# Optimization experiments

Measured on AMD Instinct MI355X. Metric: run time of the kernel, lower is better.

Reference implementation:

```python
import jax, jax.numpy as jnp
import numpy as np

NEG = -1e30  # finite stand-in for -inf padding (avoids NaN in logsumexp grads)


def _gconv(A, x, aW, ab, uW, ub):
    # Gconv: A column-normalized (L1 over dim=-2), x -> relu(a_fc(x)), relu(u_fc(x))
    An = A / jnp.maximum(jnp.sum(jnp.abs(A), axis=1, keepdims=True), 1e-12)
    ax = jax.nn.relu(x @ aW + ab)          # [B,N,D_out]
    ux = jax.nn.relu(x @ uW + ub)          # [B,N,D_out]
    return jnp.einsum('bij,bjd->bid', An, ax) + ux


def _sinkhorn(s, n1, n2, max_iter, tau):
    # log-domain Sinkhorn with ragged row/col masks (dummy_row=False, no unmatch).
    # Assumes n1[b] <= n2[b] and s.shape: [B, N1, N2] with N2 >= N1 (no transposes).
    B, N1, N2 = s.shape
    row_valid = jnp.arange(N1)[None, :] < n1[:, None]            # [B,N1]
    col_valid = jnp.arange(N2)[None, :] < n2[:, None]            # [B,N2]
    mask = row_valid[:, :, None] & col_valid[:, None, :]         # [B,N1,N2]
    log_s = jnp.where(mask, s / tau, NEG)
    for i in range(max_iter):
        if i % 2 == 0:
            lse = jax.nn.logsumexp(log_s, axis=2, keepdims=True)   # row sums
            log_s = jnp.where(row_valid[:, :, None], log_s - lse, log_s)
        else:
            lse = jax.nn.logsumexp(log_s, axis=1, keepdims=True)   # col sums
            log_s = jnp.where(col_valid[:, None, :], log_s - lse, log_s)
    return jnp.exp(jnp.where(mask, log_s, NEG))  # invalid entries -> 0


def _affinity(e1, W, e2):
    # WeightedInnerProdAffinity: e1 @ W @ e2^T
    return jnp.einsum('bid,de,bje->bij', e1, W, e2)


def setup_inputs() -> dict:
    key = jax.random.key(0)
    ks = jax.random.split(key, 20)
    B, N, IN, HID, OUT = 64, 256, 1024, 2048, 2048
    f32 = jnp.float32
    inp = {
        'feat1': jax.random.normal(ks[0], (B, N, IN), f32),
        'feat2': jax.random.normal(ks[1], (B, N, IN), f32),
        'A1': jax.random.uniform(ks[2], (B, N, N), f32),
        'A2': jax.random.uniform(ks[3], (B, N, N), f32),
        'g0_aW': jax.random.normal(ks[4], (IN, HID), f32) / np.float32(np.sqrt(IN)),
        'g0_ab': jnp.zeros((HID,), f32),
        'g0_uW': jax.random.normal(ks[5], (IN, HID), f32) / np.float32(np.sqrt(IN)),
        'g0_ub': jnp.zeros((HID,), f32),
        'g1_aW': jax.random.normal(ks[6], (HID, OUT), f32) / np.float32(np.sqrt(HID)),
        'g1_ab': jnp.zeros((OUT,), f32),
        'g1_uW': jax.random.normal(ks[7], (HID, OUT), f32) / np.float32(np.sqrt(HID)),
        'g1_ub': jnp.zeros((OUT,), f32),
        'aff0_W': jax.random.normal(ks[8], (HID, HID), f32) / np.float32(HID),
        'aff1_W': jax.random.normal(ks[9], (OUT, OUT), f32) / np.float32(OUT),
        'cross_W': jax.random.normal(ks[10], (2 * HID, HID), f32) / np.float32(np.sqrt(2 * HID)),
        'cross_b': jnp.zeros((HID,), f32),
        'n1': jax.random.randint(ks[11], (B,), 192, N + 1, jnp.int32),
        'n2': jnp.full((B,), N, jnp.int32),
        'cross_iter_num': -1,
        'sk_max_iter': 10,
        'sk_tau': 1,
    }
    return inp


def reference(feat1, feat2, A1, A2,
              g0_aW, g0_ab, g0_uW, g0_ub,
              g1_aW, g1_ab, g1_uW, g1_ub,
              aff0_W, aff1_W, cross_W, cross_b,
              n1, n2, cross_iter_num, sk_max_iter, sk_tau):
    tau = float(sk_tau)
    # layer 0 (Siamese Gconv, shared weights)
    emb1 = _gconv(A1, feat1, g0_aW, g0_ab, g0_uW, g0_ub)
    emb2 = _gconv(A2, feat2, g0_aW, g0_ab, g0_uW, g0_ub)
    # cross-graph update at i == gnn_layer - 2 (== 0 for num_layers=2)
    s = _affinity(emb1, aff0_W, emb2)
    s = _sinkhorn(s, n1, n2, sk_max_iter, tau)
    new_emb1 = jnp.concatenate([emb1, jnp.einsum('bij,bjd->bid', s, emb2)], -1) @ cross_W + cross_b
    new_emb2 = jnp.concatenate([emb2, jnp.einsum('bji,bjd->bid', s, emb1)], -1) @ cross_W + cross_b
    # layer 1 (final Siamese Gconv)
    emb1 = _gconv(A1, new_emb1, g1_aW, g1_ab, g1_uW, g1_ub)
    emb2 = _gconv(A2, new_emb2, g1_aW, g1_ab, g1_uW, g1_ub)
    s = _affinity(emb1, aff1_W, emb2)
    return _sinkhorn(s, n1, n2, sk_max_iter, tau)
```

## Files before the change

### kernel.cpp

```cpp
#include <hip/hip_runtime.h>
#include <cstdint>
#include <cstddef>

typedef __bf16 bf16;
typedef float f32x4 __attribute__((ext_vector_type(4)));
typedef bf16  bf16x8 __attribute__((ext_vector_type(8)));

#define NEGV (-1e30f)

enum { EPI_STORE = 0, EPI_ADD = 1, EPI_BIAS_RELU = 2, EPI_BIAS = 3,
       EPI_STORE_T = 5, EPI_BIAS_RELU_SCALE_T = 6, EPI_PART = 7, EPI_PARTP = 8 };

__device__ __forceinline__ void gload16(const void* g, void* l) {
    __builtin_amdgcn_global_load_lds((const __attribute__((address_space(1))) void*)g,
                                     (__attribute__((address_space(3))) void*)l, 16, 0, 0);
}

template<int EPI, typename CT, int NTJ>
__global__ __launch_bounds__(256, 2)
void hgemm_k(const bf16* __restrict__ Ab, const bf16* __restrict__ Bb,
             CT* __restrict__ Cb, const int M, const int N, const int K,
             const long long sA, const long long sB, const long long sC,
             const long long sH, const float* __restrict__ bias)
{
    __shared__ bf16 Asl[128 * 32];
    __shared__ bf16 Bsl[NTJ * 32 * 32];
    const int bz = (int)blockIdx.z;
    int ba = bz, kbeg = 0, klen = K;
    long long aoff = 0;
    if constexpr (EPI == EPI_PART) {
        ba = bz >> 3;
        const int ks = bz & 7;
        kbeg = (ks & 3) * (K >> 2); klen = K >> 2;
        aoff = (long long)(ks >> 2) * sH;
    }
    if constexpr (EPI == EPI_PARTP) {
        ba = 0; kbeg = bz * (K >> 1); klen = K >> 1;
    }
    const bf16* __restrict__ A = Ab + (long long)ba * sA + aoff;
    const bf16* __restrict__ B = Bb + (long long)ba * sB;
    CT* __restrict__ C;
    if constexpr (EPI == EPI_PART)
        C = Cb + (long long)((bz & 7) * ((int)gridDim.z >> 3) + (bz >> 3)) * sC;
    else
        C = Cb + (long long)bz * sC;

    const int m0 = blockIdx.y * 128, n0 = blockIdx.x * (NTJ * 32);
    const int tid = (int)threadIdx.x;
    const int lane = tid & 63, wave = tid >> 6;
    const int wm = (wave & 1) * 64, wn = (wave >> 1) * (NTJ * 16);
    const int lrow = lane & 15, quad = lane >> 4;

    f32x4 acc[4][NTJ];
    const f32x4 zero = {0.f, 0.f, 0.f, 0.f};
#pragma unroll
    for (int i = 0; i < 4; ++i)
#pragma unroll
        for (int j = 0; j < NTJ; ++j) acc[i][j] = zero;

    const int sr = tid >> 2, sck = (tid & 3) * 8;
    const bf16* ga0 = A + (long long)(m0 + sr) * K + kbeg + sck;
    const bf16* ga1 = ga0 + (long long)64 * K;
    const bf16* gb0 = B + (long long)(n0 + sr) * K + kbeg + sck;
    const bf16* gb1 = gb0 + (long long)64 * K;
    bf16* la0 = Asl + tid * 8;
    bf16* la1 = Asl + 2048 + tid * 8;
    bf16* lb0 = Bsl + tid * 8;
    bf16* lb1 = Bsl + 2048 + tid * 8;
    const bf16* ar = Asl + (wm + lrow) * 32 + quad * 8;
    const bf16* br = Bsl + (wn + lrow) * 32 + quad * 8;

    for (int k0 = 0; k0 < klen; k0 += 32) {
        gload16(ga0, la0); gload16(ga1, la1);
        gload16(gb0, lb0);
        if constexpr (NTJ == 4) gload16(gb1, lb1);
        ga0 += 32; ga1 += 32; gb0 += 32; gb1 += 32;
        __syncthreads();
        bf16x8 af[4], bfr[NTJ];
#pragma unroll
        for (int t = 0; t < 4; ++t) af[t] = *(const bf16x8*)(ar + t * 512);
#pragma unroll
        for (int t = 0; t < NTJ; ++t) bfr[t] = *(const bf16x8*)(br + t * 512);
#pragma unroll
        for (int i = 0; i < 4; ++i)
#pragma unroll
            for (int j = 0; j < NTJ; ++j)
                acc[i][j] = __builtin_amdgcn_mfma_f32_16x16x32_bf16(af[i], bfr[j], acc[i][j], 0, 0, 0);
        __syncthreads();
    }

#pragma unroll
    for (int ti = 0; ti < 4; ++ti) {
        const int gm0 = m0 + wm + ti * 16 + quad * 4;
#pragma unroll
        for (int r = 0; r < 4; ++r) {
            const int gm = gm0 + r;
#pragma unroll
            for (int tj = 0; tj < NTJ; ++tj) {
                const int gn = n0 + wn + tj * 16 + lrow;
                const float v = acc[ti][tj][r];
                CT* cp = C + (size_t)gm * N + gn;
                if constexpr (EPI == EPI_STORE)          *cp = (CT)v;
                else if constexpr (EPI == EPI_PART)      *cp = (CT)v;
                else if constexpr (EPI == EPI_PARTP)     *cp = (CT)v;
                else if constexpr (EPI == EPI_ADD)       *cp = (CT)((float)*cp + v);
                else if constexpr (EPI == EPI_BIAS_RELU) *cp = (CT)fmaxf(v + bias[gn], 0.f);
                else if constexpr (EPI == EPI_BIAS)      *cp = (CT)(v + bias[gn]);
            }
        }
    }
}

template<int EPI0, int EPI1, bool SWAPA0>
__global__ __launch_bounds__(256, 2)
void hgemm2_k(const bf16* __restrict__ Ab,
              const bf16* __restrict__ B0b, const bf16* __restrict__ B1b,
              bf16* __restrict__ C0b, bf16* __restrict__ C1b,
              const int M, const int N, const int K,
              const long long sA, const long long sC0, const long long sC1,
              const long long sR,
              const float* __restrict__ bias0, const float* __restrict__ bias1,
              const float* __restrict__ rowscale)
{
    __shared__ bf16 Asl[128 * 32];
    __shared__ bf16 Bsl[128 * 32];
    const int bz = (int)blockIdx.z;
    const int g = bz & 1, wsel = bz >> 1;
    const int asel = (wsel == 0 && SWAPA0) ? (g ^ 1) : g;
    const bf16* __restrict__ A = Ab + (long long)asel * sA;
    const bf16* __restrict__ B = wsel ? B1b : B0b;
    bf16* __restrict__ C = wsel ? (C1b + (long long)g * sC1)
                                : (C0b + (long long)g * sC0);
    const float* __restrict__ bias = wsel ? bias1 : bias0;
    const float* __restrict__ rs = rowscale + (long long)g * sR;

    const int m0 = blockIdx.y * 128, n0 = blockIdx.x * 128;
    const int tid = (int)threadIdx.x;
    const int lane = tid & 63, wave = tid >> 6;
    const int wm = (wave & 1) * 64, wn = (wave >> 1) * 64;
    const int lrow = lane & 15, quad = lane >> 4;

    f32x4 acc[4][4];
    const f32x4 zero = {0.f, 0.f, 0.f, 0.f};
#pragma unroll
    for (int i = 0; i < 4; ++i)
#pragma unroll
        for (int j = 0; j < 4; ++j) acc[i][j] = zero;

    const int sr = tid >> 2, sck = (tid & 3) * 8;
    const bf16* ga0 = A + (long long)(m0 + sr) * K + sck;
    const bf16* ga1 = ga0 + (long long)64 * K;
    const bf16* gb0 = B + (long long)(n0 + sr) * K + sck;
    const bf16* gb1 = gb0 + (long long)64 * K;
    bf16* la0 = Asl + tid * 8;
    bf16* la1 = Asl + 2048 + tid * 8;
    bf16* lb0 = Bsl + tid * 8;
    bf16* lb1 = Bsl + 2048 + tid * 8;
    const bf16* ar = Asl + (wm + lrow) * 32 + quad * 8;
    const bf16* br = Bsl + (wn + lrow) * 32 + quad * 8;

    for (int k0 = 0; k0 < K; k0 += 32) {
        gload16(ga0, la0); gload16(ga1, la1);
        gload16(gb0, lb0); gload16(gb1, lb1);
        ga0 += 32; ga1 += 32; gb0 += 32; gb1 += 32;
        __syncthreads();
        bf16x8 af[4], bfr[4];
#pragma unroll
        for (int t = 0; t < 4; ++t) {
            af[t]  = *(const bf16x8*)(ar + t * 512);
            bfr[t] = *(const bf16x8*)(br + t * 512);
        }
#pragma unroll
        for (int i = 0; i < 4; ++i)
#pragma unroll
            for (int j = 0; j < 4; ++j)
                acc[i][j] = __builtin_amdgcn_mfma_f32_16x16x32_bf16(af[i], bfr[j], acc[i][j], 0, 0, 0);
        __syncthreads();
    }

    if (wsel == 0) {
#pragma unroll
        for (int ti = 0; ti < 4; ++ti) {
            const int gm0 = m0 + wm + ti * 16 + quad * 4;
#pragma unroll
            for (int tj = 0; tj < 4; ++tj) {
                const int gn = n0 + wn + tj * 16 + lrow;
                union { bf16 h[4]; uint2 u; } p;
#pragma unroll
                for (int r = 0; r < 4; ++r) {
                    float v = acc[ti][tj][r];
                    if constexpr (EPI0 == EPI_BIAS_RELU_SCALE_T)
                        v = fmaxf(v + bias[gn], 0.f) * rs[gm0 + r];
                    p.h[r] = (bf16)v;
                }
                *(uint2*)(C + ((size_t)(gm0 >> 8)) * 524288 +
                          (size_t)gn * 256 + (gm0 & 255)) = p.u;
            }
        }
    } else {
#pragma unroll
        for (int ti = 0; ti < 4; ++ti) {
            const int gm0 = m0 + wm + ti * 16 + quad * 4;
#pragma unroll
            for (int r = 0; r < 4; ++r) {
                const int gm = gm0 + r;
#pragma unroll
                for (int tj = 0; tj < 4; ++tj) {
                    const int gn = n0 + wn + tj * 16 + lrow;
                    const float v = acc[ti][tj][r];
                    bf16* cp = C + (size_t)gm * N + gn;
                    if constexpr (EPI1 == EPI_BIAS_RELU) *cp = (bf16)fmaxf(v + bias[gn], 0.f);
                    else                                 *cp = (bf16)(v + bias[gn]);
                }
            }
        }
    }
}

__global__ __launch_bounds__(256)
void wtrans_k(const float* __restrict__ W, bf16* __restrict__ Wt, const int K, const int N)
{
    __shared__ float tl[32][33];
    const int k0 = blockIdx.y * 32, n0 = blockIdx.x * 32;
    const int tx = (int)threadIdx.x & 31, ty = (int)threadIdx.x >> 5;
#pragma unroll
    for (int q = 0; q < 4; ++q)
        tl[ty + 8 * q][tx] = W[(size_t)(k0 + ty + 8 * q) * N + n0 + tx];
    __syncthreads();
#pragma unroll
    for (int q = 0; q < 4; ++q)
        Wt[(size_t)(n0 + ty + 8 * q) * K + k0 + tx] = (bf16)tl[tx][ty + 8 * q];
}

__global__ __launch_bounds__(256)
void cvt_k(const float4* __restrict__ in, uint2* __restrict__ out, const long long n4)
{
    long long i = (long long)blockIdx.x * 256 + threadIdx.x;
    const long long st = (long long)gridDim.x * 256;
    for (; i < n4; i += st) {
        const float4 v = in[i];
        union { bf16 h[4]; uint2 u; } p;
        p.h[0] = (bf16)v.x; p.h[1] = (bf16)v.y; p.h[2] = (bf16)v.z; p.h[3] = (bf16)v.w;
        out[i] = p.u;
    }
}

__global__ __launch_bounds__(256)
void colsum_rcp_k(const float* __restrict__ A, float* __restrict__ rcs,
                  const int nbl2, const int g)
{
    const int b = blockIdx.x, j = (int)threadIdx.x;
    const int cch = b >> nbl2, ii = b & ((1 << nbl2) - 1), nb = 1 << nbl2;
    const float* p = A + (size_t)b * 65536;
    float s = 0.f;
    for (int i = 0; i < 256; ++i) s += fabsf(p[i * 256 + j]);
    rcs[(size_t)((cch * 2 + g) * nb + ii) * 256 + j] = 1.f / fmaxf(s, 1e-12f);
}

__global__ __launch_bounds__(256)
void mask_tau_red_k(const float* __restrict__ Sp, float* __restrict__ S,
                    const int* __restrict__ n1p, const int* __restrict__ n2p,
                    const int* __restrict__ taup, const int nb)
{
    const size_t t = (size_t)blockIdx.x * 256 + threadIdx.x;
    const int b = (int)(t >> 16), i = (int)((t >> 8) & 255), j = (int)(t & 255);
    const size_t stride = (size_t)nb << 16;
    float s = 0.f;
#pragma unroll
    for (int ks = 0; ks < 8; ++ks) s += Sp[ks * stride + t];
    const float tau = (float)taup[0];
    S[t] = (i < n1p[b] && j < n2p[b]) ? s / tau : NEGV;
}

template<int WRITE_SB>
__global__ __launch_bounds__(1024, 4)
void sk_fused_k(float* __restrict__ S, bf16* __restrict__ S2b,
                const int* __restrict__ n1p, const int* __restrict__ n2p,
                const int nbl2)
{
    __shared__ float lm[32][256];
    __shared__ float lp[4][256];
    __shared__ float lf[256];
    const int b = (int)blockIdx.x;
    const int tid = (int)threadIdx.x;
    const int a = tid >> 5, bb = tid & 31;
    const int r0 = a * 8, c0 = bb * 8;
    const int n1 = n1p[b], n2 = n2p[b];
    float* Sb_ = S + ((size_t)b << 16);

    float v[8][8];
#pragma unroll
    for (int ri = 0; ri < 8; ++ri) {
        const float4* rp = (const float4*)(Sb_ + (size_t)(r0 + ri) * 256 + c0);
        const float4 x0 = rp[0], x1 = rp[1];
        v[ri][0] = x0.x; v[ri][1] = x0.y; v[ri][2] = x0.z; v[ri][3] = x0.w;
        v[ri][4] = x1.x; v[ri][5] = x1.y; v[ri][6] = x1.z; v[ri][7] = x1.w;
    }

    for (int it = 0; it < 10; ++it) {
        if ((it & 1) == 0) {
#pragma unroll
            for (int ri = 0; ri < 8; ++ri) {
                float m = v[ri][0];
#pragma unroll
                for (int c = 1; c < 8; ++c) m = fmaxf(m, v[ri][c]);
#pragma unroll
                for (int off = 1; off < 32; off <<= 1) m = fmaxf(m, __shfl_xor(m, off));
                float s = 0.f;
#pragma unroll
                for (int c = 0; c < 8; ++c) s += expf(v[ri][c] - m);
#pragma unroll
                for (int off = 1; off < 32; off <<= 1) s += __shfl_xor(s, off);
                const float lse = m + logf(s);
                if (r0 + ri < n1) {
#pragma unroll
                    for (int c = 0; c < 8; ++c) v[ri][c] -= lse;
                }
            }
        } else {
            __syncthreads();
#pragma unroll
            for (int c = 0; c < 8; ++c) {
                float m = v[0][c];
#pragma unroll
                for (int ri = 1; ri < 8; ++ri) m = fmaxf(m, v[ri][c]);
                lm[a][c0 + c] = m;
            }
            __syncthreads();
            {
                const int jt = tid & 255, qt = tid >> 8;
                float m = lm[qt * 8][jt];
#pragma unroll
                for (int aa = 1; aa < 8; ++aa) m = fmaxf(m, lm[qt * 8 + aa][jt]);
                lp[qt][jt] = m;
            }
            __syncthreads();
            if (tid < 256)
                lf[tid] = fmaxf(fmaxf(lp[0][tid], lp[1][tid]),
                                fmaxf(lp[2][tid], lp[3][tid]));
            __syncthreads();
            float M[8];
#pragma unroll
            for (int c = 0; c < 8; ++c) M[c] = lf[c0 + c];
            __syncthreads();
#pragma unroll
            for (int c = 0; c < 8; ++c) {
                float s = 0.f;
#pragma unroll
                for (int ri = 0; ri < 8; ++ri) s += expf(v[ri][c] - M[c]);
                lm[a][c0 + c] = s;
            }
            __syncthreads();
            {
                const int jt = tid & 255, qt = tid >> 8;
                float s = 0.f;
#pragma unroll
                for (int aa = 0; aa < 8; ++aa) s += lm[qt * 8 + aa][jt];
                lp[qt][jt] = s;
            }
            __syncthreads();
            if (tid < 256)
                lf[tid] = lf[tid] + logf(lp[0][tid] + lp[1][tid] + lp[2][tid] + lp[3][tid]);
            __syncthreads();
#pragma unroll
            for (int c = 0; c < 8; ++c) {
                if (c0 + c < n2) {
                    const float lse = lf[c0 + c];
#pragma unroll
                    for (int ri = 0; ri < 8; ++ri) v[ri][c] -= lse;
                }
            }
        }
    }

#pragma unroll
    for (int ri = 0; ri < 8; ++ri)
#pragma unroll
        for (int c = 0; c < 8; ++c)
            v[ri][c] = (r0 + ri < n1 && c0 + c < n2) ? expf(v[ri][c]) : 0.f;

    if constexpr (WRITE_SB) {
        const int nb = 1 << nbl2;
        const int cch = b >> nbl2, ii = b & (nb - 1);
        bf16* sbB = S2b + ((size_t)((cch * 2) * nb + ii) << 16);
        bf16* stB = S2b + ((size_t)((cch * 2 + 1) * nb + ii) << 16);
#pragma unroll
        for (int ri = 0; ri < 8; ++ri) {
            union { bf16 h[8]; uint4 u; } p;
#pragma unroll
            for (int c = 0; c < 8; ++c) p.h[c] = (bf16)v[ri][c];
            *(uint4*)(sbB + (size_t)(r0 + ri) * 256 + c0) = p.u;
        }
#pragma unroll
        for (int c = 0; c < 8; ++c) {
            union { bf16 h[8]; uint4 u; } p;
#pragma unroll
            for (int ri = 0; ri < 8; ++ri) p.h[ri] = (bf16)v[ri][c];
            *(uint4*)(stB + (size_t)(c0 + c) * 256 + r0) = p.u;
        }
    } else {
#pragma unroll
        for (int ri = 0; ri < 8; ++ri) {
            float4 x0, x1;
            x0.x = v[ri][0]; x0.y = v[ri][1]; x0.z = v[ri][2]; x0.w = v[ri][3];
            x1.x = v[ri][4]; x1.y = v[ri][5]; x1.z = v[ri][6]; x1.w = v[ri][7];
            float4* rp = (float4*)(Sb_ + (size_t)(r0 + ri) * 256 + c0);
            rp[0] = x0; rp[1] = x1;
        }
    }
}

extern "C" void kernel_launch(void* const* d_in, const int* in_sizes, int n_in,
                              void* d_out, int out_size, void* d_ws, size_t ws_size,
                              hipStream_t stream)
{
    (void)in_sizes; (void)n_in; (void)out_size;
    const float* feat1  = (const float*)d_in[0];
    const float* feat2  = (const float*)d_in[1];
    const float* A1     = (const float*)d_in[2];
    const float* A2     = (const float*)d_in[3];
    const float* g0_aW  = (const float*)d_in[4];
    const float* g0_ab  = (const float*)d_in[5];
    const float* g0_uW  = (const float*)d_in[6];
    const float* g0_ub  = (const float*)d_in[7];
    const float* g1_aW  = (const float*)d_in[8];
    const float* g1_ab  = (const float*)d_in[9];
    const float* g1_uW  = (const float*)d_in[10];
    const float* g1_ub  = (const float*)d_in[11];
    const float* aff0_W = (const float*)d_in[12];
    const float* aff1_W = (const float*)d_in[13];
    const float* cross_W = (const float*)d_in[14];
    const float* cross_b = (const float*)d_in[15];
    const int* n1p = (const int*)d_in[16];
    const int* n2p = (const int*)d_in[17];
    const int* taup = (const int*)d_in[20];

    float* S = (float*)d_out;

    bf16* w = (bf16*)d_ws;
    bf16* E12b = w;   w += 67108864;
    bf16* g0aWt = w;  w += 2097152;
    bf16* g0uWt = w;  w += 2097152;
    bf16* g1aWt = w;  w += 4194304;
    bf16* g1uWt = w;  w += 4194304;
    bf16* aff0Wt = w; w += 4194304;
    bf16* aff1Wt = w; w += 4194304;
    bf16* cWtT = w;   w += 4194304;
    bf16* cWbT = w;   w += 4194304;
    bf16* A12b = w;   w += 8388608;
    bf16* S2b = w;    w += 8388608;
    float* rcs_cg = (float*)w; w += 65536;

    int nb = 1;
    {
        const long long avail = (long long)ws_size - 226623488LL;
        while (nb < 32 && (long long)(nb * 2) * 4194304LL <= avail) nb <<= 1;
    }
    const int nbl2 = __builtin_ctz(nb);
    const int nc = 64 / nb;
    bf16* Ha = w;
    bf16* region2 = Ha + (size_t)2 * nb * 524288;
    bf16* Fbc2 = region2;
    bf16* H12 = region2;
    float* Spart = (float*)region2;

    const dim3 blk(256);
    const dim3 gF2(16, nb * 2, 4);
    const dim3 gAdd(16, 2, nb * 2);
    const dim3 gP(32, nb * 2, 2);
    const dim3 gPart(4, 2, nb * 8);

    const long long EC = (long long)nb * 524288;
    const long long FC = (long long)nb * 262144;
    const long long PH = (long long)nb * 524288;

    wtrans_k<<<dim3(64, 32), blk, 0, stream>>>(g0_aW, g0aWt, 1024, 2048);
    wtrans_k<<<dim3(64, 32), blk, 0, stream>>>(g0_uW, g0uWt, 1024, 2048);
    wtrans_k<<<dim3(64, 64), blk, 0, stream>>>(g1_aW, g1aWt, 2048, 2048);
    wtrans_k<<<dim3(64, 64), blk, 0, stream>>>(g1_uW, g1uWt, 2048, 2048);
    wtrans_k<<<dim3(64, 64), blk, 0, stream>>>(aff0_W, aff0Wt, 2048, 2048);
    wtrans_k<<<dim3(64, 64), blk, 0, stream>>>(aff1_W, aff1Wt, 2048, 2048);
    wtrans_k<<<dim3(64, 64), blk, 0, stream>>>(cross_W, cWtT, 2048, 2048);
    wtrans_k<<<dim3(64, 64), blk, 0, stream>>>(cross_W + 4194304, cWbT, 2048, 2048);
    for (int c = 0; c < nc; ++c) {
        cvt_k<<<256, blk, 0, stream>>>((const float4*)(A1 + (long long)c * nb * 65536),
                                       (uint2*)(A12b + (long long)c * 2 * nb * 65536),
                                       (long long)nb * 16384);
        cvt_k<<<256, blk, 0, stream>>>((const float4*)(A2 + (long long)c * nb * 65536),
                                       (uint2*)(A12b + (long long)(c * 2 + 1) * nb * 65536),
                                       (long long)nb * 16384);
    }
    colsum_rcp_k<<<64, blk, 0, stream>>>(A1, rcs_cg, nbl2, 0);
    colsum_rcp_k<<<64, blk, 0, stream>>>(A2, rcs_cg, nbl2, 1);

    for (int c = 0; c < nc; ++c) {
        bf16* E12c = E12b + (long long)c * 2 * EC;
        const float* rsc = rcs_cg + (long long)c * 2 * nb * 256;
        cvt_k<<<1024, blk, 0, stream>>>((const float4*)(feat1 + (long long)c * nb * 262144),
                                        (uint2*)Fbc2, (long long)nb * 65536);
        cvt_k<<<1024, blk, 0, stream>>>((const float4*)(feat2 + (long long)c * nb * 262144),
                                        (uint2*)(Fbc2 + FC), (long long)nb * 65536);
        hgemm2_k<EPI_BIAS_RELU_SCALE_T, EPI_BIAS_RELU, false><<<gF2, blk, 0, stream>>>(
            Fbc2, g0aWt, g0uWt, Ha, E12c, nb * 256, 2048, 1024,
            FC, EC, EC, nb * 256, g0_ab, g0_ub, rsc);
        hgemm_k<EPI_ADD, bf16, 4><<<gAdd, blk, 0, stream>>>(
            A12b + (long long)c * 2 * nb * 65536, Ha, E12c, 256, 2048, 256,
            65536, 524288, 524288, 0, nullptr);
        hgemm_k<EPI_PARTP, bf16, 2><<<gP, blk, 0, stream>>>(
            E12c, aff0Wt, Ha, nb * 256, 2048, 2048, 0, 0, PH, 0, nullptr);
        hgemm_k<EPI_PART, float, 2><<<gPart, blk, 0, stream>>>(
            Ha, E12c + EC, Spart, 256, 256, 2048, 524288, 524288, 65536, PH, nullptr);
        mask_tau_red_k<<<nb * 256, blk, 0, stream>>>(
            Spart, S + (long long)c * nb * 65536, n1p + c * nb, n2p + c * nb, taup, nb);
    }
    sk_fused_k<1><<<64, dim3(1024), 0, stream>>>(S, S2b, n1p, n2p, nbl2);

    for (int c = 0; c < nc; ++c) {
        bf16* E12c = E12b + (long long)c * 2 * EC;
        const float* rsc = rcs_cg + (long long)c * 2 * nb * 256;
        hgemm2_k<EPI_STORE_T, EPI_BIAS, true><<<gF2, blk, 0, stream>>>(
            E12c, cWbT, cWtT, Ha, H12, nb * 256, 2048, 2048,
            EC, EC, EC, 0, nullptr, cross_b, nullptr);
        hgemm_k<EPI_ADD, bf16, 4><<<gAdd, blk, 0, stream>>>(
            S2b + (long long)c * 2 * nb * 65536, Ha, H12, 256, 2048, 256,
            65536, 524288, 524288, 0, nullptr);
        hgemm2_k<EPI_BIAS_RELU_SCALE_T, EPI_BIAS_RELU, false><<<gF2, blk, 0, stream>>>(
            H12, g1aWt, g1uWt, Ha, E12c, nb * 256, 2048, 2048,
            EC, EC, EC, nb * 256, g1_ab, g1_ub, rsc);
        hgemm_k<EPI_ADD, bf16, 4><<<gAdd, blk, 0, stream>>>(
            A12b + (long long)c * 2 * nb * 65536, Ha, E12c, 256, 2048, 256,
            65536, 524288, 524288, 0, nullptr);
        hgemm_k<EPI_PARTP, bf16, 2><<<gP, blk, 0, stream>>>(
            E12c, aff1Wt, Ha, nb * 256, 2048, 2048, 0, 0, PH, 0, nullptr);
        hgemm_k<EPI_PART, float, 2><<<gPart, blk, 0, stream>>>(
            Ha, E12c + EC, Spart, 256, 256, 2048, 524288, 524288, 65536, PH, nullptr);
        mask_tau_red_k<<<nb * 256, blk, 0, stream>>>(
            Spart, S + (long long)c * nb * 65536, n1p + c * nb, n2p + c * nb, taup, nb);
    }
    sk_fused_k<0><<<64, dim3(1024), 0, stream>>>(S, nullptr, n1p, n2p, 0);
}
```

Baseline: 3.543 ms.

## Split Sinkhorn over four blocks per batch with grid sync; add XCD swizzle

The fused Sinkhorn kernel used to run one 1024-thread block per batch (64 blocks), leaving most CUs idle. It now runs as a cooperative kernel with four blocks per batch, each holding 64 rows. Column log-sum-exp uses an online (max, sum) merge written to a global scratch buffer and combined after grid.sync(). Separately, all GEMM kernels remap block indices so that consecutive tiles land on the same XCD, to improve L2 locality. Risks: grid-wide sync cost per column iteration, and colred aliases region2, which other stages also use as scratch.

```diff
diff --git a/kernel.cpp b/kernel.cpp
--- a/kernel.cpp
+++ b/kernel.cpp
@@ -1,6 +1,9 @@
 #include <hip/hip_runtime.h>
+#include <hip/hip_cooperative_groups.h>
 #include <cstdint>
 #include <cstddef>
+
+namespace cg = cooperative_groups;
 
 typedef __bf16 bf16;
 typedef float f32x4 __attribute__((ext_vector_type(4)));
@@ -14,6 +17,17 @@
 __device__ __forceinline__ void gload16(const void* g, void* l) {
     __builtin_amdgcn_global_load_lds((const __attribute__((address_space(1))) void*)g,
                                      (__attribute__((address_space(3))) void*)l, 16, 0, 0);
+}
+
+__device__ __forceinline__ void xcd_swz(int& bx, int& by, int& bz) {
+    const int gx = (int)gridDim.x, gy = (int)gridDim.y, gz = (int)gridDim.z;
+    const int nwg = gx * gy * gz;
+    const int lid = (bz * gy + by) * gx + bx;
+    const int q = nwg >> 3, r = nwg & 7;
+    const int xcd = lid & 7, idx = lid >> 3;
+    int swz = (xcd < r ? xcd * (q + 1) : r * (q + 1) + (xcd - r) * q) + idx;
+    bx = swz % gx; swz /= gx;
+    by = swz % gy; bz = swz / gy;
 }
 
 template<int EPI, typename CT, int NTJ>
@@ -25,7 +39,9 @@
 {
     __shared__ bf16 Asl[128 * 32];
     __shared__ bf16 Bsl[NTJ * 32 * 32];
-    const int bz = (int)blockIdx.z;
+    int bxs = (int)blockIdx.x, bys = (int)blockIdx.y, bzs = (int)blockIdx.z;
+    xcd_swz(bxs, bys, bzs);
+    const int bz = bzs;
     int ba = bz, kbeg = 0, klen = K;
     long long aoff = 0;
     if constexpr (EPI == EPI_PART) {
@@ -45,7 +61,7 @@
     else
         C = Cb + (long long)bz * sC;
 
-    const int m0 = blockIdx.y * 128, n0 = blockIdx.x * (NTJ * 32);
+    const int m0 = bys * 128, n0 = bxs * (NTJ * 32);
     const int tid = (int)threadIdx.x;
     const int lane = tid & 63, wave = tid >> 6;
     const int wm = (wave & 1) * 64, wn = (wave >> 1) * (NTJ * 16);
@@ -124,7 +140,9 @@
 {
     __shared__ bf16 Asl[128 * 32];
     __shared__ bf16 Bsl[128 * 32];
-    const int bz = (int)blockIdx.z;
+    int bxs = (int)blockIdx.x, bys = (int)blockIdx.y, bzs = (int)blockIdx.z;
+    xcd_swz(bxs, bys, bzs);
+    const int bz = bzs;
     const int g = bz & 1, wsel = bz >> 1;
     const int asel = (wsel == 0 && SWAPA0) ? (g ^ 1) : g;
     const bf16* __restrict__ A = Ab + (long long)asel * sA;
@@ -134,7 +152,7 @@
     const float* __restrict__ bias = wsel ? bias1 : bias0;
     const float* __restrict__ rs = rowscale + (long long)g * sR;
 
-    const int m0 = blockIdx.y * 128, n0 = blockIdx.x * 128;
+    const int m0 = bys * 128, n0 = bxs * 128;
     const int tid = (int)threadIdx.x;
     const int lane = tid & 63, wave = tid >> 6;
     const int wm = (wave & 1) * 64, wn = (wave >> 1) * 64;
@@ -272,25 +290,32 @@
     S[t] = (i < n1p[b] && j < n2p[b]) ? s / tau : NEGV;
 }
 
+__device__ __forceinline__ float2 lse_comb(float2 x, float2 y) {
+    const float M = fmaxf(x.x, y.x);
+    float2 r; r.x = M; r.y = x.y * expf(x.x - M) + y.y * expf(y.x - M);
+    return r;
+}
+
 template<int WRITE_SB>
-__global__ __launch_bounds__(1024, 4)
-void sk_fused_k(float* __restrict__ S, bf16* __restrict__ S2b,
-                const int* __restrict__ n1p, const int* __restrict__ n2p,
-                const int nbl2)
-{
-    __shared__ float lm[32][256];
-    __shared__ float lp[4][256];
-    __shared__ float lf[256];
-    const int b = (int)blockIdx.x;
+__global__ __launch_bounds__(1024)
+void sk_coop_k(float* __restrict__ S, bf16* __restrict__ S2b,
+               float2* __restrict__ colred,
+               const int* __restrict__ n1p, const int* __restrict__ n2p,
+               const int nbl2)
+{
+    __shared__ float2 lw[16][256];
+    cg::grid_group grid = cg::this_grid();
+    const int bid = (int)blockIdx.x;
+    const int b = bid >> 2, q = bid & 3;
     const int tid = (int)threadIdx.x;
     const int a = tid >> 5, bb = tid & 31;
-    const int r0 = a * 8, c0 = bb * 8;
+    const int r0 = q * 64 + a * 2, c0 = bb * 8;
     const int n1 = n1p[b], n2 = n2p[b];
     float* Sb_ = S + ((size_t)b << 16);
 
-    float v[8][8];
-#pragma unroll
-    for (int ri = 0; ri < 8; ++ri) {
+    float v[2][8];
+#pragma unroll
+    for (int ri = 0; ri < 2; ++ri) {
         const float4* rp = (const float4*)(Sb_ + (size_t)(r0 + ri) * 256 + c0);
         const float4 x0 = rp[0], x1 = rp[1];
         v[ri][0] = x0.x; v[ri][1] = x0.y; v[ri][2] = x0.z; v[ri][3] = x0.w;
@@ -300,7 +325,7 @@
     for (int it = 0; it < 10; ++it) {
         if ((it & 1) == 0) {
 #pragma unroll
-            for (int ri = 0; ri < 8; ++ri) {
+            for (int ri = 0; ri < 2; ++ri) {
                 float m = v[ri][0];
 #pragma unroll
                 for (int c = 1; c < 8; ++c) m = fmaxf(m, v[ri][c]);
@@ -318,63 +343,49 @@
                 }
             }
         } else {
+            const int par = (it >> 1) & 1;
+            float2 loc[8];
+#pragma unroll
+            for (int c = 0; c < 8; ++c) {
+                const float m = fmaxf(v[0][c], v[1][c]);
+                loc[c].x = m;
+                loc[c].y = expf(v[0][c] - m) + expf(v[1][c] - m);
+            }
+#pragma unroll
+            for (int c = 0; c < 8; ++c) {
+                float2 o;
+                o.x = __shfl_xor(loc[c].x, 32);
+                o.y = __shfl_xor(loc[c].y, 32);
+                loc[c] = lse_comb(loc[c], o);
+            }
+            if ((tid & 63) < 32) {
+                const int wv = tid >> 6;
+#pragma unroll
+                for (int c = 0; c < 8; ++c) lw[wv][c0 + c] = loc[c];
+            }
             __syncthreads();
+            if (tid < 256) {
+                float2 acc = lw[0][tid];
+#pragma unroll
+                for (int wv = 1; wv < 16; ++wv) acc = lse_comb(acc, lw[wv][tid]);
+                colred[(((size_t)par * 64 + b) * 4 + q) * 256 + tid] = acc;
+            }
+            grid.sync();
+            const float2* cr = colred + (((size_t)par * 64 + b) * 4) * 256;
 #pragma unroll
             for (int c = 0; c < 8; ++c) {
-                float m = v[0][c];
-#pragma unroll
-                for (int ri = 1; ri < 8; ++ri) m = fmaxf(m, v[ri][c]);
-                lm[a][c0 + c] = m;
-            }
-            __syncthreads();
-            {
-                const int jt = tid & 255, qt = tid >> 8;
-                float m = lm[qt * 8][jt];
-#pragma unroll
-                for (int aa = 1; aa < 8; ++aa) m = fmaxf(m, lm[qt * 8 + aa][jt]);
-                lp[qt][jt] = m;
-            }
-            __syncthreads();
-            if (tid < 256)
-                lf[tid] = fmaxf(fmaxf(lp[0][tid], lp[1][tid]),
-                                fmaxf(lp[2][tid], lp[3][tid]));
-            __syncthreads();
-            float M[8];
-#pragma unroll
-            for (int c = 0; c < 8; ++c) M[c] = lf[c0 + c];
-            __syncthreads();
-#pragma unroll
-            for (int c = 0; c < 8; ++c) {
-                float s = 0.f;
-#pragma unroll
-                for (int ri = 0; ri < 8; ++ri) s += expf(v[ri][c] - M[c]);
-                lm[a][c0 + c] = s;
-            }
-            __syncthreads();
-            {
-                const int jt = tid & 255, qt = tid >> 8;
-                float s = 0.f;
-#pragma unroll
-                for (int aa = 0; aa < 8; ++aa) s += lm[qt * 8 + aa][jt];
-                lp[qt][jt] = s;
-            }
-            __syncthreads();
-            if (tid < 256)
-                lf[tid] = lf[tid] + logf(lp[0][tid] + lp[1][tid] + lp[2][tid] + lp[3][tid]);
-            __syncthreads();
-#pragma unroll
-            for (int c = 0; c < 8; ++c) {
-                if (c0 + c < n2) {
-                    const float lse = lf[c0 + c];
-#pragma unroll
-                    for (int ri = 0; ri < 8; ++ri) v[ri][c] -= lse;
-                }
-            }
-        }
-    }
-
-#pragma unroll
-    for (int ri = 0; ri < 8; ++ri)
+                float2 acc = cr[c0 + c];
+                acc = lse_comb(acc, cr[256 + c0 + c]);
+                acc = lse_comb(acc, cr[512 + c0 + c]);
+                acc = lse_comb(acc, cr[768 + c0 + c]);
+                const float lse = acc.x + logf(acc.y);
+                if (c0 + c < n2) { v[0][c] -= lse; v[1][c] -= lse; }
+            }
+        }
+    }
+
+#pragma unroll
+    for (int ri = 0; ri < 2; ++ri)
 #pragma unroll
         for (int c = 0; c < 8; ++c)
             v[ri][c] = (r0 + ri < n1 && c0 + c < n2) ? expf(v[ri][c]) : 0.f;
@@ -385,7 +396,7 @@
         bf16* sbB = S2b + ((size_t)((cch * 2) * nb + ii) << 16);
         bf16* stB = S2b + ((size_t)((cch * 2 + 1) * nb + ii) << 16);
 #pragma unroll
-        for (int ri = 0; ri < 8; ++ri) {
+        for (int ri = 0; ri < 2; ++ri) {
             union { bf16 h[8]; uint4 u; } p;
 #pragma unroll
             for (int c = 0; c < 8; ++c) p.h[c] = (bf16)v[ri][c];
@@ -393,14 +404,13 @@
         }
 #pragma unroll
         for (int c = 0; c < 8; ++c) {
-            union { bf16 h[8]; uint4 u; } p;
-#pragma unroll
-            for (int ri = 0; ri < 8; ++ri) p.h[ri] = (bf16)v[ri][c];
-            *(uint4*)(stB + (size_t)(c0 + c) * 256 + r0) = p.u;
+            union { bf16 h[2]; unsigned u; } p;
+            p.h[0] = (bf16)v[0][c]; p.h[1] = (bf16)v[1][c];
+            *(unsigned*)(stB + (size_t)(c0 + c) * 256 + r0) = p.u;
         }
     } else {
 #pragma unroll
-        for (int ri = 0; ri < 8; ++ri) {
+        for (int ri = 0; ri < 2; ++ri) {
             float4 x0, x1;
             x0.x = v[ri][0]; x0.y = v[ri][1]; x0.z = v[ri][2]; x0.w = v[ri][3];
             x1.x = v[ri][4]; x1.y = v[ri][5]; x1.z = v[ri][6]; x1.w = v[ri][7];
@@ -463,6 +473,7 @@
     bf16* Fbc2 = region2;
     bf16* H12 = region2;
     float* Spart = (float*)region2;
+    float2* colred = (float2*)region2;
 
     const dim3 blk(256);
     const dim3 gF2(16, nb * 2, 4);
@@ -513,7 +524,14 @@
         mask_tau_red_k<<<nb * 256, blk, 0, stream>>>(
             Spart, S + (long long)c * nb * 65536, n1p + c * nb, n2p + c * nb, taup, nb);
     }
-    sk_fused_k<1><<<64, dim3(1024), 0, stream>>>(S, S2b, n1p, n2p, nbl2);
+    {
+        float* S_ = S; bf16* S2b_ = S2b; float2* cr_ = colred;
+        const int* n1_ = n1p; const int* n2_ = n2p; int nbl2_ = nbl2;
+        void* args[6] = { &S_, &S2b_, &cr_, &n1_, &n2_, &nbl2_ };
+        void (*fp)(float*, bf16*, float2*, const int*, const int*, int) = sk_coop_k<1>;
+        hipLaunchCooperativeKernel(reinterpret_cast<const void*>(fp),
+                                   dim3(256), dim3(1024), args, 0, stream);
+    }
 
     for (int c = 0; c < nc; ++c) {
         bf16* E12c = E12b + (long long)c * 2 * EC;
@@ -537,5 +555,12 @@
         mask_tau_red_k<<<nb * 256, blk, 0, stream>>>(
             Spart, S + (long long)c * nb * 65536, n1p + c * nb, n2p + c * nb, taup, nb);
     }
-    sk_fused_k<0><<<64, dim3(1024), 0, stream>>>(S, nullptr, n1p, n2p, 0);
-}
+    {
+        float* S_ = S; bf16* S2b_ = nullptr; float2* cr_ = colred;
+        const int* n1_ = n1p; const int* n2_ = n2p; int nbl2_ = 0;
+        void* args[6] = { &S_, &S2b_, &cr_, &n1_, &n2_, &nbl2_ };
+        void (*fp)(float*, bf16*, float2*, const int*, const int*, int) = sk_coop_k<0>;
+        hipLaunchCooperativeKernel(reinterpret_cast<const void*>(fp),
+                                   dim3(256), dim3(1024), args, 0, stream);
+    }
+}
```

New measurement: 3.758 ms. +6.1%, slower.

## Split fused Sinkhorn into multi-block row/column kernels with fused first row step

Applied to the files above, without the earlier changes.

Replaces the single-block-per-batch fused Sinkhorn kernel (64 blocks of 1024 threads, all 10 iterations in registers) with a sequence of smaller kernels. The partial-sum reduction, masking and tau scaling now also do the first row normalization. Then four column/row kernel pairs run, and a final column kernel applies the exp, the mask and the bf16 or transposed writes. The aim is to spread Sinkhorn over many more blocks than 64 for better GPU occupancy. The cost is extra kernel launches and a full read-write of S through global memory on every iteration.

```diff
diff --git a/kernel.cpp b/kernel.cpp
--- a/kernel.cpp
+++ b/kernel.cpp
@@ -257,156 +257,164 @@
     rcs[(size_t)((cch * 2 + g) * nb + ii) * 256 + j] = 1.f / fmaxf(s, 1e-12f);
 }
 
-__global__ __launch_bounds__(256)
-void mask_tau_red_k(const float* __restrict__ Sp, float* __restrict__ S,
-                    const int* __restrict__ n1p, const int* __restrict__ n2p,
-                    const int* __restrict__ taup, const int nb)
-{
-    const size_t t = (size_t)blockIdx.x * 256 + threadIdx.x;
-    const int b = (int)(t >> 16), i = (int)((t >> 8) & 255), j = (int)(t & 255);
+__device__ __forceinline__ float2 lse_comb(float2 x, float2 y) {
+    const float M = fmaxf(x.x, y.x);
+    float2 r; r.x = M; r.y = x.y * expf(x.x - M) + y.y * expf(y.x - M);
+    return r;
+}
+
+__global__ __launch_bounds__(256)
+void sk_mrow_k(const float* __restrict__ Sp, float* __restrict__ S,
+               const int* __restrict__ n1p, const int* __restrict__ n2p,
+               const int* __restrict__ taup, const int nb)
+{
+    const int w = (int)threadIdx.x >> 6, lane = (int)threadIdx.x & 63;
+    const int rowg = blockIdx.x * 4 + w;
+    const int b = rowg >> 8, i = rowg & 255;
+    const int n1 = n1p[b], n2 = n2p[b];
+    const float tau = (float)taup[0];
     const size_t stride = (size_t)nb << 16;
+    const size_t base = (size_t)rowg * 256 + (size_t)lane * 4;
+    float4 s4 = {0.f, 0.f, 0.f, 0.f};
+#pragma unroll
+    for (int ks = 0; ks < 8; ++ks) {
+        const float4 t = *(const float4*)(Sp + ks * stride + base);
+        s4.x += t.x; s4.y += t.y; s4.z += t.z; s4.w += t.w;
+    }
+    const int j0 = lane * 4;
+    float4 v;
+    v.x = (i < n1 && j0 + 0 < n2) ? s4.x / tau : NEGV;
+    v.y = (i < n1 && j0 + 1 < n2) ? s4.y / tau : NEGV;
+    v.z = (i < n1 && j0 + 2 < n2) ? s4.z / tau : NEGV;
+    v.w = (i < n1 && j0 + 3 < n2) ? s4.w / tau : NEGV;
+    float m = fmaxf(fmaxf(v.x, v.y), fmaxf(v.z, v.w));
+#pragma unroll
+    for (int off = 32; off > 0; off >>= 1) m = fmaxf(m, __shfl_down(m, off));
+    m = __shfl(m, 0);
+    float s = expf(v.x - m) + expf(v.y - m) + expf(v.z - m) + expf(v.w - m);
+#pragma unroll
+    for (int off = 32; off > 0; off >>= 1) s += __shfl_down(s, off);
+    s = __shfl(s, 0);
+    const float lse = m + logf(s);
+    if (i < n1) { v.x -= lse; v.y -= lse; v.z -= lse; v.w -= lse; }
+    *(float4*)(S + base) = v;
+}
+
+__global__ __launch_bounds__(256)
+void sk_row_k(float* __restrict__ S, const int* __restrict__ n1p)
+{
+    const int w = (int)threadIdx.x >> 6, lane = (int)threadIdx.x & 63;
+    const int rowg = blockIdx.x * 4 + w;
+    const int b = rowg >> 8, i = rowg & 255;
+    float* p = S + (size_t)rowg * 256;
+    float4 v = ((const float4*)p)[lane];
+    float m = fmaxf(fmaxf(v.x, v.y), fmaxf(v.z, v.w));
+#pragma unroll
+    for (int off = 32; off > 0; off >>= 1) m = fmaxf(m, __shfl_down(m, off));
+    m = __shfl(m, 0);
+    float s = expf(v.x - m) + expf(v.y - m) + expf(v.z - m) + expf(v.w - m);
+#pragma unroll
+    for (int off = 32; off > 0; off >>= 1) s += __shfl_down(s, off);
+    s = __shfl(s, 0);
+    const float lse = m + logf(s);
+    if (i < n1p[b]) {
+        v.x -= lse; v.y -= lse; v.z -= lse; v.w -= lse;
+        ((float4*)p)[lane] = v;
+    }
+}
+
+__global__ __launch_bounds__(256)
+void sk_col2_k(float* __restrict__ S, const int* __restrict__ n2p)
+{
+    __shared__ float2 part[4][64];
+    __shared__ float lsev[64];
+    const int bid = (int)blockIdx.x;
+    const int b = bid >> 2, c0 = (bid & 3) * 64;
+    const int t = (int)threadIdx.x, j = c0 + (t & 63), q = t >> 6;
+    float* base = S + ((size_t)b << 16) + (size_t)q * 16384 + j;
+    float v[64];
+#pragma unroll
+    for (int i = 0; i < 64; ++i) v[i] = base[i * 256];
+    float m = v[0];
+#pragma unroll
+    for (int i = 1; i < 64; ++i) m = fmaxf(m, v[i]);
     float s = 0.f;
 #pragma unroll
-    for (int ks = 0; ks < 8; ++ks) s += Sp[ks * stride + t];
-    const float tau = (float)taup[0];
-    S[t] = (i < n1p[b] && j < n2p[b]) ? s / tau : NEGV;
+    for (int i = 0; i < 64; ++i) s += expf(v[i] - m);
+    part[q][t & 63] = make_float2(m, s);
+    __syncthreads();
+    if (t < 64) {
+        float2 a = part[0][t];
+        a = lse_comb(a, part[1][t]);
+        a = lse_comb(a, part[2][t]);
+        a = lse_comb(a, part[3][t]);
+        lsev[t] = a.x + logf(a.y);
+    }
+    __syncthreads();
+    if (j < n2p[b]) {
+        const float l = lsev[t & 63];
+#pragma unroll
+        for (int i = 0; i < 64; ++i) base[i * 256] = v[i] - l;
+    }
 }
 
 template<int WRITE_SB>
-__global__ __launch_bounds__(1024, 4)
-void sk_fused_k(float* __restrict__ S, bf16* __restrict__ S2b,
-                const int* __restrict__ n1p, const int* __restrict__ n2p,
-                const int nbl2)
-{
-    __shared__ float lm[32][256];
-    __shared__ float lp[4][256];
-    __shared__ float lf[256];
-    const int b = (int)blockIdx.x;
-    const int tid = (int)threadIdx.x;
-    const int a = tid >> 5, bb = tid & 31;
-    const int r0 = a * 8, c0 = bb * 8;
-    const int n1 = n1p[b], n2 = n2p[b];
-    float* Sb_ = S + ((size_t)b << 16);
-
-    float v[8][8];
-#pragma unroll
-    for (int ri = 0; ri < 8; ++ri) {
-        const float4* rp = (const float4*)(Sb_ + (size_t)(r0 + ri) * 256 + c0);
-        const float4 x0 = rp[0], x1 = rp[1];
-        v[ri][0] = x0.x; v[ri][1] = x0.y; v[ri][2] = x0.z; v[ri][3] = x0.w;
-        v[ri][4] = x1.x; v[ri][5] = x1.y; v[ri][6] = x1.z; v[ri][7] = x1.w;
-    }
-
-    for (int it = 0; it < 10; ++it) {
-        if ((it & 1) == 0) {
-#pragma unroll
-            for (int ri = 0; ri < 8; ++ri) {
-                float m = v[ri][0];
-#pragma unroll
-                for (int c = 1; c < 8; ++c) m = fmaxf(m, v[ri][c]);
-#pragma unroll
-                for (int off = 1; off < 32; off <<= 1) m = fmaxf(m, __shfl_xor(m, off));
-                float s = 0.f;
-#pragma unroll
-                for (int c = 0; c < 8; ++c) s += expf(v[ri][c] - m);
-#pragma unroll
-                for (int off = 1; off < 32; off <<= 1) s += __shfl_xor(s, off);
-                const float lse = m + logf(s);
-                if (r0 + ri < n1) {
-#pragma unroll
-                    for (int c = 0; c < 8; ++c) v[ri][c] -= lse;
-                }
-            }
-        } else {
-            __syncthreads();
-#pragma unroll
-            for (int c = 0; c < 8; ++c) {
-                float m = v[0][c];
-#pragma unroll
-                for (int ri = 1; ri < 8; ++ri) m = fmaxf(m, v[ri][c]);
-                lm[a][c0 + c] = m;
-            }
-            __syncthreads();
-            {
-                const int jt = tid & 255, qt = tid >> 8;
-                float m = lm[qt * 8][jt];
-#pragma unroll
-                for (int aa = 1; aa < 8; ++aa) m = fmaxf(m, lm[qt * 8 + aa][jt]);
-                lp[qt][jt] = m;
-            }
-            __syncthreads();
-            if (tid < 256)
-                lf[tid] = fmaxf(fmaxf(lp[0][tid], lp[1][tid]),
-                                fmaxf(lp[2][tid], lp[3][tid]));
-            __syncthreads();
-            float M[8];
-#pragma unroll
-            for (int c = 0; c < 8; ++c) M[c] = lf[c0 + c];
-            __syncthreads();
-#pragma unroll
-            for (int c = 0; c < 8; ++c) {
-                float s = 0.f;
-#pragma unroll
-                for (int ri = 0; ri < 8; ++ri) s += expf(v[ri][c] - M[c]);
-                lm[a][c0 + c] = s;
-            }
-            __syncthreads();
-            {
-                const int jt = tid & 255, qt = tid >> 8;
-                float s = 0.f;
-#pragma unroll
-                for (int aa = 0; aa < 8; ++aa) s += lm[qt * 8 + aa][jt];
-                lp[qt][jt] = s;
-            }
-            __syncthreads();
-            if (tid < 256)
-                lf[tid] = lf[tid] + logf(lp[0][tid] + lp[1][tid] + lp[2][tid] + lp[3][tid]);
-            __syncthreads();
-#pragma unroll
-            for (int c = 0; c < 8; ++c) {
-                if (c0 + c < n2) {
-                    const float lse = lf[c0 + c];
-#pragma unroll
-                    for (int ri = 0; ri < 8; ++ri) v[ri][c] -= lse;
-                }
-            }
-        }
-    }
-
-#pragma unroll
-    for (int ri = 0; ri < 8; ++ri)
-#pragma unroll
-        for (int c = 0; c < 8; ++c)
-            v[ri][c] = (r0 + ri < n1 && c0 + c < n2) ? expf(v[ri][c]) : 0.f;
-
+__global__ __launch_bounds__(256)
+void sk_fin_k(float* __restrict__ S, bf16* __restrict__ S2b,
+              const int* __restrict__ n1p, const int* __restrict__ n2p,
+              const int nbl2)
+{
+    __shared__ float2 part[4][64];
+    __shared__ float lsev[64];
+    const int bid = (int)blockIdx.x;
+    const int b = bid >> 2, c0 = (bid & 3) * 64;
+    const int t = (int)threadIdx.x, j = c0 + (t & 63), q = t >> 6;
+    float* base = S + ((size_t)b << 16) + (size_t)q * 16384 + j;
+    float v[64];
+#pragma unroll
+    for (int i = 0; i < 64; ++i) v[i] = base[i * 256];
+    float m = v[0];
+#pragma unroll
+    for (int i = 1; i < 64; ++i) m = fmaxf(m, v[i]);
+    float s = 0.f;
+#pragma unroll
+    for (int i = 0; i < 64; ++i) s += expf(v[i] - m);
+    part[q][t & 63] = make_float2(m, s);
+    __syncthreads();
+    if (t < 64) {
+        float2 a = part[0][t];
+        a = lse_comb(a, part[1][t]);
+        a = lse_comb(a, part[2][t]);
+        a = lse_comb(a, part[3][t]);
+        lsev[t] = a.x + logf(a.y);
+    }
+    __syncthreads();
+    const int n1 = n1p[b];
+    const bool jv = j < n2p[b];
+    const float l = jv ? lsev[t & 63] : 0.f;
+#pragma unroll
+    for (int i = 0; i < 64; ++i) {
+        const int row = q * 64 + i;
+        v[i] = (row < n1 && jv) ? expf(v[i] - l) : 0.f;
+    }
     if constexpr (WRITE_SB) {
         const int nb = 1 << nbl2;
         const int cch = b >> nbl2, ii = b & (nb - 1);
         bf16* sbB = S2b + ((size_t)((cch * 2) * nb + ii) << 16);
         bf16* stB = S2b + ((size_t)((cch * 2 + 1) * nb + ii) << 16);
 #pragma unroll
-        for (int ri = 0; ri < 8; ++ri) {
-            union { bf16 h[8]; uint4 u; } p;
-#pragma unroll
-            for (int c = 0; c < 8; ++c) p.h[c] = (bf16)v[ri][c];
-            *(uint4*)(sbB + (size_t)(r0 + ri) * 256 + c0) = p.u;
-        }
-#pragma unroll
-        for (int c = 0; c < 8; ++c) {
-            union { bf16 h[8]; uint4 u; } p;
-#pragma unroll
-            for (int ri = 0; ri < 8; ++ri) p.h[ri] = (bf16)v[ri][c];
-            *(uint4*)(stB + (size_t)(c0 + c) * 256 + r0) = p.u;
+        for (int i = 0; i < 64; ++i)
+            sbB[(size_t)(q * 64 + i) * 256 + j] = (bf16)v[i];
+#pragma unroll
+        for (int w8 = 0; w8 < 8; ++w8) {
+            union { bf16 h[8]; uint4 uu; } pk;
+#pragma unroll
+            for (int e = 0; e < 8; ++e) pk.h[e] = (bf16)v[w8 * 8 + e];
+            *(uint4*)(stB + (size_t)j * 256 + q * 64 + w8 * 8) = pk.uu;
         }
     } else {
 #pragma unroll
-        for (int ri = 0; ri < 8; ++ri) {
-            float4 x0, x1;
-            x0.x = v[ri][0]; x0.y = v[ri][1]; x0.z = v[ri][2]; x0.w = v[ri][3];
-            x1.x = v[ri][4]; x1.y = v[ri][5]; x1.z = v[ri][6]; x1.w = v[ri][7];
-            float4* rp = (float4*)(Sb_ + (size_t)(r0 + ri) * 256 + c0);
-            rp[0] = x0; rp[1] = x1;
-        }
+        for (int i = 0; i < 64; ++i) base[i * 256] = v[i];
     }
 }
 
@@ -510,10 +518,14 @@
             E12c, aff0Wt, Ha, nb * 256, 2048, 2048, 0, 0, PH, 0, nullptr);
         hgemm_k<EPI_PART, float, 2><<<gPart, blk, 0, stream>>>(
             Ha, E12c + EC, Spart, 256, 256, 2048, 524288, 524288, 65536, PH, nullptr);
-        mask_tau_red_k<<<nb * 256, blk, 0, stream>>>(
+        sk_mrow_k<<<nb * 64, blk, 0, stream>>>(
             Spart, S + (long long)c * nb * 65536, n1p + c * nb, n2p + c * nb, taup, nb);
     }
-    sk_fused_k<1><<<64, dim3(1024), 0, stream>>>(S, S2b, n1p, n2p, nbl2);
+    for (int p = 0; p < 4; ++p) {
+        sk_col2_k<<<256, blk, 0, stream>>>(S, n2p);
+        sk_row_k<<<4096, blk, 0, stream>>>(S, n1p);
+    }
+    sk_fin_k<1><<<256, blk, 0, stream>>>(S, S2b, n1p, n2p, nbl2);
 
     for (int c = 0; c < nc; ++c) {
         bf16* E12c = E12b + (long long)c * 2 * EC;
@@ -534,8 +546,12 @@
             E12c, aff1Wt, Ha, nb * 256, 2048, 2048, 0, 0, PH, 0, nullptr);
         hgemm_k<EPI_PART, float, 2><<<gPart, blk, 0, stream>>>(
             Ha, E12c + EC, Spart, 256, 256, 2048, 524288, 524288, 65536, PH, nullptr);
-        mask_tau_red_k<<<nb * 256, blk, 0, stream>>>(
+        sk_mrow_k<<<nb * 64, blk, 0, stream>>>(
             Spart, S + (long long)c * nb * 65536, n1p + c * nb, n2p + c * nb, taup, nb);
     }
-    sk_fused_k<0><<<64, dim3(1024), 0, stream>>>(S, nullptr, n1p, n2p, 0);
-}
+    for (int p = 0; p < 4; ++p) {
+        sk_col2_k<<<256, blk, 0, stream>>>(S, n2p);
+        sk_row_k<<<4096, blk, 0, stream>>>(S, n1p);
+    }
+    sk_fin_k<0><<<256, blk, 0, stream>>>(S, nullptr, n1p, n2p, 0);
+}
```

Measured after the change: 3.473 ms. 2.0% less time.
